# Optimization experiments

Measured on AMD Instinct MI355X. Metric: run time of the kernel, lower is better.

## Reference

```python
import jax, jax.numpy as jnp
import numpy as np

FEAT = 256
HID = 256
HEADS = 4
DH = HID // HEADS
SCALE = DH ** (-0.5)


def _linear(x, W, b):
    # torch nn.Linear convention: W is [out, in]
    return jnp.einsum('...i,oi->...o', x, W) + b


def _layernorm(x, gamma, beta, eps=1e-5):
    mu = jnp.mean(x, axis=-1, keepdims=True)
    var = jnp.mean(jnp.square(x - mu), axis=-1, keepdims=True)
    return (x - mu) * jax.lax.rsqrt(var + eps) * gamma + beta


def setup_inputs() -> dict:
    key = jax.random.key(0)
    ks = jax.random.split(key, 16)
    B, N = 4, 2048
    def w(k, shape, fan_in):
        return jax.random.uniform(k, shape, jnp.float32, -1.0, 1.0) / np.sqrt(fan_in)
    return {
        'x0': jax.random.normal(ks[0], (B, N, FEAT), jnp.float32),
        'x1': jax.random.normal(ks[1], (B, N, FEAT), jnp.float32),
        'Wqk': w(ks[2], (HID, FEAT), FEAT), 'bqk': w(ks[3], (HID,), FEAT),
        'Wv': w(ks[4], (HID, FEAT), FEAT), 'bv': w(ks[5], (HID,), FEAT),
        'Wp': w(ks[6], (HID, HID), HID), 'bp': w(ks[7], (HID,), HID),
        'W1': w(ks[8], (FEAT * 2, FEAT + HID), FEAT + HID), 'b1': w(ks[9], (FEAT * 2,), FEAT + HID),
        'gamma': jnp.ones((FEAT * 2,), jnp.float32), 'beta': jnp.zeros((FEAT * 2,), jnp.float32),
        'W2': w(ks[10], (FEAT, FEAT * 2), FEAT * 2), 'b2': w(ks[11], (FEAT,), FEAT * 2),
    }


def _forward(x0, x1, Wqk, bqk, Wv, bv, Wp, bp, W1, b1, gamma, beta, W2, b2):
    B, N0, _ = x0.shape
    N1 = x1.shape[1]

    def heads(t):  # [B, N, HID] -> [B, H, N, DH]
        return t.reshape(t.shape[0], t.shape[1], HEADS, DH).transpose(0, 2, 1, 3)

    qk0 = heads(_linear(x0, Wqk, bqk)) * (SCALE ** 0.5)
    qk1 = heads(_linear(x1, Wqk, bqk)) * (SCALE ** 0.5)
    v0 = heads(_linear(x0, Wv, bv))
    v1 = heads(_linear(x1, Wv, bv))

    sim = jnp.einsum('bhid,bhjd->bhij', qk0, qk1)  # [B,H,N0,N1]
    attn01 = jax.nn.softmax(sim, axis=-1)                      # rows over N1
    attn10 = jax.nn.softmax(sim.transpose(0, 1, 3, 2), axis=-1)  # [B,H,N1,N0], rows over N0

    m0 = jnp.einsum('bhij,bhjd->bhid', attn01, v1)  # [B,H,N0,DH]
    m1 = jnp.einsum('bhij,bhjd->bhid', attn10, v0)  # [B,H,N1,DH]

    def merge(t):  # [B,H,N,DH] -> [B,N,HID]
        return t.transpose(0, 2, 1, 3).reshape(t.shape[0], t.shape[2], HID)

    m0 = _linear(merge(m0), Wp, bp)
    m1 = _linear(merge(m1), Wp, bp)

    def mlp(x, m):
        h = _linear(jnp.concatenate([x, m], axis=-1), W1, b1)
        h = jax.nn.gelu(_layernorm(h, gamma, beta), approximate=False)
        return x + _linear(h, W2, b2)

    return mlp(x0, m0), mlp(x1, m1)


def reference(x0, x1, Wqk, bqk, Wv, bv, Wp, bp, W1, b1, gamma, beta, W2, b2):
    return _forward(x0, x1, Wqk, bqk, Wv, bv, Wp, bp, W1, b1, gamma, beta, W2, b2)
```

## Files before the change

### kernel.cpp

```cpp
#include <hip/hip_runtime.h>
#include <hip/hip_bf16.h>
#include <math.h>

typedef __hip_bfloat16 hbf;
typedef __attribute__((ext_vector_type(8))) short short8;
typedef __attribute__((ext_vector_type(4))) short short4v;
typedef __attribute__((ext_vector_type(4))) float f32x4;

#define ROWS 8192
#define SQSL 0.4246609001440095f
#define COFF 24.0f

__device__ __forceinline__ short f2b(float f) {
    union { hbf h; short s; } u; u.h = __float2bfloat16(f); return u.s;
}
__device__ __forceinline__ float b2f(short s) {
    union { unsigned u; float f; } x;
    x.u = ((unsigned)(unsigned short)s) << 16; return x.f;
}

__global__ __launch_bounds__(256)
void prep(const float* __restrict__ x0, const float* __restrict__ x1,
          const float* __restrict__ Wqk, const float* __restrict__ Wv,
          const float* __restrict__ Wp, const float* __restrict__ W1,
          const float* __restrict__ W2,
          const float* __restrict__ bp, const float* __restrict__ b1,
          short* __restrict__ xbf, short* __restrict__ wq,
          short* __restrict__ wv, short* __restrict__ w1c,
          short* __restrict__ w2, float* __restrict__ bc)
{
    const int bid = blockIdx.x, tid = threadIdx.x;
    if (bid < 4608) {
        if (bid >= 4224 && bid < 4480) {
            int i = (bid - 4224) * 256 + tid;
            int n = i >> 7, c = (i & 127) * 4;
            if (c < 256) {
                float4 f = ((const float4*)W1)[i];
                short4v s;
                s[0] = f2b(f.x); s[1] = f2b(f.y); s[2] = f2b(f.z); s[3] = f2b(f.w);
                *(short4v*)(w1c + (size_t)n * 512 + c) = s;
            }
            return;
        }
        const float* src; short* dst; int base; float sc = 1.f;
        if (bid < 2048)      { src = x0;  dst = xbf;              base = bid; }
        else if (bid < 4096) { src = x1;  dst = xbf + 8192 * 256; base = bid - 2048; }
        else if (bid < 4160) { src = Wqk; dst = wq; base = bid - 4096; sc = SQSL; }
        else if (bid < 4224) { src = Wv;  dst = wv; base = bid - 4160; }
        else                 { src = W2;  dst = w2; base = bid - 4480; }
        int i = base * 256 + tid;
        float4 f = ((const float4*)src)[i];
        short4v s;
        s[0] = f2b(f.x * sc); s[1] = f2b(f.y * sc);
        s[2] = f2b(f.z * sc); s[3] = f2b(f.w * sc);
        *(short4v*)(dst + (size_t)i * 4) = s;
    } else if (bid < 5120) {
        int n = bid - 4608;
        const float* wrow = W1 + (size_t)n * 512 + 256;
        float acc = 0.f;
        for (int k = 0; k < 256; ++k)
            acc += wrow[k] * Wp[(size_t)k * 256 + tid];
        w1c[(size_t)n * 512 + 256 + tid] = f2b(acc);
    } else {
        int n = (bid - 5120) * 256 + tid;
        const float* wrow = W1 + (size_t)n * 512 + 256;
        float acc = b1[n];
        for (int k = 0; k < 256; ++k) acc += wrow[k] * bp[k];
        bc[n] = acc;
    }
}

__global__ __launch_bounds__(256)
void gemm_qkv(const short* __restrict__ A0,
              const short* __restrict__ Wa, const short* __restrict__ Wb,
              const float* __restrict__ bias0, const float* __restrict__ bias1,
              short* __restrict__ Cb, short* __restrict__ Cb2)
{
    const int col0 = blockIdx.x * 128;
    const int row0 = blockIdx.y * 64;
    const int tid = threadIdx.x;
    const int lane = tid & 63, wave = tid >> 6;
    const int ln = lane & 15, quad = lane >> 4;
    const int wm = wave & 1, wn = wave >> 1;

    __shared__ short As[64 * 40];
    __shared__ short Bs[128 * 40];

    const int ar = tid >> 2, ac = tid & 3;

    f32x4 acc[2][4];
    #pragma unroll
    for (int i = 0; i < 2; ++i)
        #pragma unroll
        for (int j = 0; j < 4; ++j) acc[i][j] = {0.f, 0.f, 0.f, 0.f};

    auto wptr = [&](int rr, int kk) -> const short* {
        int n = col0 + rr;
        if (col0 < 256) return Wa + (size_t)n * 256 + kk;
        return Wb + (size_t)(n - 256) * 256 + kk;
    };

    short8 aR  = *(const short8*)(A0 + (size_t)(row0 + ar) * 256 + ac * 8);
    short8 bR0 = *(const short8*)wptr(ar, ac * 8);
    short8 bR1 = *(const short8*)wptr(ar + 64, ac * 8);

    for (int k0 = 0; k0 < 256; k0 += 32) {
        *(short8*)&As[ar * 40 + ac * 8] = aR;
        *(short8*)&Bs[ar * 40 + ac * 8] = bR0;
        *(short8*)&Bs[(ar + 64) * 40 + ac * 8] = bR1;
        __syncthreads();

        if (k0 + 32 < 256) {
            aR  = *(const short8*)(A0 + (size_t)(row0 + ar) * 256 + k0 + 32 + ac * 8);
            bR0 = *(const short8*)wptr(ar, k0 + 32 + ac * 8);
            bR1 = *(const short8*)wptr(ar + 64, k0 + 32 + ac * 8);
        }

        short8 a[2], b[4];
        #pragma unroll
        for (int mi = 0; mi < 2; ++mi)
            a[mi] = *(const short8*)&As[(wm * 32 + mi * 16 + ln) * 40 + quad * 8];
        #pragma unroll
        for (int nj = 0; nj < 4; ++nj)
            b[nj] = *(const short8*)&Bs[(wn * 64 + nj * 16 + ln) * 40 + quad * 8];
        #pragma unroll
        for (int mi = 0; mi < 2; ++mi)
            #pragma unroll
            for (int nj = 0; nj < 4; ++nj)
                acc[mi][nj] = __builtin_amdgcn_mfma_f32_16x16x32_bf16(
                                  b[nj], a[mi], acc[mi][nj], 0, 0, 0);
        __syncthreads();
    }

    #pragma unroll
    for (int nj = 0; nj < 4; ++nj) {
        int wrel = wn * 64 + nj * 16 + quad * 4;
        int wcol = col0 + wrel;
        const float* bias = (wcol >= 256) ? bias1 : bias0;
        int boff = (wcol >= 256) ? (wcol - 256) : wcol;
        float4 bb = *(const float4*)(bias + boff);
        #pragma unroll
        for (int mi = 0; mi < 2; ++mi) {
            int tok = row0 + wm * 32 + mi * 16 + ln;
            f32x4 v = acc[mi][nj];
            short4v o;
            if (wcol < 256) {
                o[0] = f2b(fmaf(bb.x, SQSL, v[0])); o[1] = f2b(fmaf(bb.y, SQSL, v[1]));
                o[2] = f2b(fmaf(bb.z, SQSL, v[2])); o[3] = f2b(fmaf(bb.w, SQSL, v[3]));
                *(short4v*)(Cb + (size_t)tok * 256 + wcol) = o;
            } else {
                o[0] = f2b(v[0] + bb.x); o[1] = f2b(v[1] + bb.y);
                o[2] = f2b(v[2] + bb.z); o[3] = f2b(v[3] + bb.w);
                *(short4v*)(Cb2 + (size_t)tok * 256 + (wcol - 256)) = o;
            }
        }
    }
}

__global__ __launch_bounds__(256)
void vtrans(const short* __restrict__ vbuf, short* __restrict__ vtbuf)
{
    const int tt = blockIdx.x;
    const int gh = blockIdx.y;
    const int g = gh >> 2, h = gh & 3;
    const int tid = threadIdx.x;
    const int tok0 = g * 2048 + tt * 64;

    __shared__ short Ls[64 * 76];

    {
        int c4 = tid & 15, r0 = tid >> 4;
        #pragma unroll
        for (int gg = 0; gg < 4; ++gg) {
            int r = r0 + gg * 16;
            *(short4v*)&Ls[r * 76 + c4 * 4] =
                *(const short4v*)(vbuf + (size_t)(tok0 + r) * 256 + h * 64 + c4 * 4);
        }
    }
    __syncthreads();

    #pragma unroll
    for (int p = 0; p < 2; ++p) {
        int ch = tid + p * 256;
        int d = ch >> 3, cc = ch & 7;
        short8 s;
        #pragma unroll
        for (int j = 0; j < 8; ++j) s[j] = Ls[(cc * 8 + j) * 76 + d];
        *(short8*)(vtbuf + (size_t)((g * 4 + h) * 64 + d) * 2048 + tt * 64 + cc * 8) = s;
    }
}

__global__ __launch_bounds__(256)
void attn7(const short* __restrict__ qkb, const short* __restrict__ vtbuf,
           short* __restrict__ pO0, short* __restrict__ pO1,
           float* __restrict__ l0, float* __restrict__ l1)
{
    const int qt   = blockIdx.x;
    const int b    = blockIdx.y >> 2, h = blockIdx.y & 3;
    const int dir  = blockIdx.z >> 1;
    const int half = blockIdx.z & 1;
    const int tid = threadIdx.x;
    const int lane = tid & 63, wave = tid >> 6;
    const int ln   = lane & 15, quad = lane >> 4;

    const int qbase = dir * ROWS + b * 2048;
    const int kbase = (1 - dir) * ROWS + b * 2048;
    const int vg    = ((1 - dir) * 4 + b) * 4 + h;
    const int jlo   = half * 1024, jhi = jlo + 1024;

    short* __restrict__ pO = half ? pO1 : pO0;
    float* __restrict__ lb = half ? l1  : l0;

    __shared__ short QP[128 * 72];
    __shared__ short KS[64 * 72];
    __shared__ short VT[64 * 72];

    const int c = tid & 7, r0 = tid >> 3;
    #pragma unroll
    for (int g = 0; g < 4; ++g) {
        int r = r0 + g * 32;
        *(short8*)&QP[r * 72 + c * 8] =
            *(const short8*)(qkb + (size_t)(qbase + qt * 128 + r) * 256 + h * 64 + c * 8);
    }
    #pragma unroll
    for (int g = 0; g < 2; ++g) {
        int r = r0 + g * 32;
        *(short8*)&KS[r * 72 + c * 8] =
            *(const short8*)(qkb + (size_t)(kbase + jlo + r) * 256 + h * 64 + c * 8);
        *(short8*)&VT[r * 72 + c * 8] =
            *(const short8*)(vtbuf + (size_t)(vg * 64 + r) * 2048 + jlo + c * 8);
    }
    __syncthreads();

    short8 qf[2][2];
    #pragma unroll
    for (int mi = 0; mi < 2; ++mi)
        #pragma unroll
        for (int ks = 0; ks < 2; ++ks)
            qf[mi][ks] = *(const short8*)&QP[(wave * 32 + mi * 16 + ln) * 72
                                             + ks * 32 + quad * 8];

    f32x4 Ot[2][4];
    #pragma unroll
    for (int mi = 0; mi < 2; ++mi)
        #pragma unroll
        for (int dt = 0; dt < 4; ++dt) Ot[mi][dt] = {0.f, 0.f, 0.f, 0.f};
    float lrun[2] = {0.f, 0.f};

    for (int j0 = jlo; j0 < jhi; j0 += 64) {
        short8 kreg[2], vreg[2];
        const bool more = (j0 + 64) < jhi;
        if (more) {
            #pragma unroll
            for (int g = 0; g < 2; ++g) {
                int r = r0 + g * 32;
                kreg[g] = *(const short8*)(qkb + (size_t)(kbase + j0 + 64 + r) * 256
                                           + h * 64 + c * 8);
                vreg[g] = *(const short8*)(vtbuf + (size_t)(vg * 64 + r) * 2048
                                           + j0 + 64 + c * 8);
            }
        }

        f32x4 St[2][4];
        #pragma unroll
        for (int t = 0; t < 4; ++t) {
            short8 k0 = *(const short8*)&KS[(t * 16 + ln) * 72 + quad * 8];
            short8 k1 = *(const short8*)&KS[(t * 16 + ln) * 72 + 32 + quad * 8];
            #pragma unroll
            for (int mi = 0; mi < 2; ++mi) {
                f32x4 z = {0.f, 0.f, 0.f, 0.f};
                z = __builtin_amdgcn_mfma_f32_16x16x32_bf16(k0, qf[mi][0], z, 0, 0, 0);
                St[mi][t] = __builtin_amdgcn_mfma_f32_16x16x32_bf16(k1, qf[mi][1], z, 0, 0, 0);
            }
        }

        float ss[2] = {0.f, 0.f};
        #pragma unroll
        for (int mi = 0; mi < 2; ++mi)
            #pragma unroll
            for (int t = 0; t < 4; ++t) {
                float p0 = __builtin_amdgcn_exp2f(St[mi][t][0] - COFF);
                float p1 = __builtin_amdgcn_exp2f(St[mi][t][1] - COFF);
                float p2 = __builtin_amdgcn_exp2f(St[mi][t][2] - COFF);
                float p3 = __builtin_amdgcn_exp2f(St[mi][t][3] - COFF);
                ss[mi] += (p0 + p1) + (p2 + p3);
                unsigned d0 = (__float_as_uint(p0) >> 16) |
                              (__float_as_uint(p1) & 0xffff0000u);
                unsigned d1 = (__float_as_uint(p2) >> 16) |
                              (__float_as_uint(p3) & 0xffff0000u);
                *(int2*)&QP[(wave * 32 + mi * 16 + ln) * 72 + t * 16 + quad * 4] =
                    make_int2((int)d0, (int)d1);
            }
        #pragma unroll
        for (int mi = 0; mi < 2; ++mi) {
            float t = ss[mi];
            t += __shfl_xor(t, 16);
            t += __shfl_xor(t, 32);
            lrun[mi] += t;
        }

        short8 pa[2][2];
        #pragma unroll
        for (int mi = 0; mi < 2; ++mi)
            #pragma unroll
            for (int ks = 0; ks < 2; ++ks)
                pa[mi][ks] = *(const short8*)&QP[(wave * 32 + mi * 16 + ln) * 72
                                                 + ks * 32 + quad * 8];
        #pragma unroll
        for (int dt = 0; dt < 4; ++dt) {
            short8 v0 = *(const short8*)&VT[(dt * 16 + ln) * 72 + quad * 8];
            short8 v1 = *(const short8*)&VT[(dt * 16 + ln) * 72 + 32 + quad * 8];
            #pragma unroll
            for (int mi = 0; mi < 2; ++mi) {
                Ot[mi][dt] = __builtin_amdgcn_mfma_f32_16x16x32_bf16(
                                 v0, pa[mi][0], Ot[mi][dt], 0, 0, 0);
                Ot[mi][dt] = __builtin_amdgcn_mfma_f32_16x16x32_bf16(
                                 v1, pa[mi][1], Ot[mi][dt], 0, 0, 0);
            }
        }
        __syncthreads();

        if (more) {
            #pragma unroll
            for (int g = 0; g < 2; ++g) {
                int r = r0 + g * 32;
                *(short8*)&KS[r * 72 + c * 8] = kreg[g];
                *(short8*)&VT[r * 72 + c * 8] = vreg[g];
            }
        }
        __syncthreads();
    }

    #pragma unroll
    for (int mi = 0; mi < 2; ++mi) {
        int tok = qbase + qt * 128 + wave * 32 + mi * 16 + ln;
        if (quad == 0) lb[tok] = lrun[mi];
        #pragma unroll
        for (int dt = 0; dt < 4; ++dt) {
            short4v o;
            #pragma unroll
            for (int r = 0; r < 4; ++r) o[r] = f2b(Ot[mi][dt][r]);
            *(short4v*)(pO + (size_t)tok * 256 + h * 64 + dt * 16 + quad * 4) = o;
        }
    }
}

__global__ __launch_bounds__(256)
void mlp_fused(const short* __restrict__ xbf,
               const short* __restrict__ pO0, const short* __restrict__ pO1,
               const float* __restrict__ l0, const float* __restrict__ l1,
               const short* __restrict__ w1c, const short* __restrict__ w2,
               const float* __restrict__ bc, const float* __restrict__ gamma,
               const float* __restrict__ beta, const float* __restrict__ b2,
               const float* __restrict__ x0, const float* __restrict__ x1,
               float* __restrict__ out)
{
    const int tok0 = blockIdx.x * 32;
    const int tid = threadIdx.x;
    const int lane = tid & 63, wave = tid >> 6;
    const int ln = lane & 15, quad = lane >> 4;

    __shared__ short As[32 * 40];
    __shared__ short Bs[256 * 40];
    __shared__ short H [32 * 520];
    __shared__ float stats[4][2][32];

    f32x4 acc[2][8];
    #pragma unroll
    for (int i = 0; i < 2; ++i)
        #pragma unroll
        for (int j = 0; j < 8; ++j) acc[i][j] = {0.f, 0.f, 0.f, 0.f};

    const int br = tid >> 2, bcol = tid & 3;

    for (int k0 = 0; k0 < 512; k0 += 32) {
        #pragma unroll
        for (int p = 0; p < 2; ++p) {
            if (p == 0 && tid < 128) {
                int arow = tid >> 2, ac = tid & 3;
                int kk = k0 + ac * 8;
                int tok = tok0 + arow;
                short8 s;
                if (k0 < 256) {
                    s = *(const short8*)(xbf + (size_t)tok * 256 + kk);
                } else {
                    short8 a = *(const short8*)(pO0 + (size_t)tok * 256 + (kk - 256));
                    short8 b = *(const short8*)(pO1 + (size_t)tok * 256 + (kk - 256));
                    float inv = __builtin_amdgcn_rcpf(l0[tok] + l1[tok]);
                    #pragma unroll
                    for (int j = 0; j < 8; ++j)
                        s[j] = f2b((b2f(a[j]) + b2f(b[j])) * inv);
                }
                *(short8*)&As[arow * 40 + ac * 8] = s;
            }
            #pragma unroll
            for (int q = 0; q < 4; ++q) {
                int r = br + q * 64;
                *(short8*)&Bs[r * 40 + bcol * 8] =
                    *(const short8*)(w1c + (size_t)(p * 256 + r) * 512 + k0 + bcol * 8);
            }
            __syncthreads();

            short8 a0 = *(const short8*)&As[ln * 40 + quad * 8];
            short8 a1 = *(const short8*)&As[(16 + ln) * 40 + quad * 8];
            #pragma unroll
            for (int nj = 0; nj < 4; ++nj) {
                short8 bf = *(const short8*)&Bs[(wave * 64 + nj * 16 + ln) * 40 + quad * 8];
                acc[0][p * 4 + nj] = __builtin_amdgcn_mfma_f32_16x16x32_bf16(
                                         bf, a0, acc[0][p * 4 + nj], 0, 0, 0);
                acc[1][p * 4 + nj] = __builtin_amdgcn_mfma_f32_16x16x32_bf16(
                                         bf, a1, acc[1][p * 4 + nj], 0, 0, 0);
            }
            __syncthreads();
        }
    }

    #pragma unroll
    for (int p = 0; p < 2; ++p)
        #pragma unroll
        for (int nj = 0; nj < 4; ++nj) {
            int hcol = p * 256 + wave * 64 + nj * 16 + quad * 4;
            float4 bb = *(const float4*)(bc + hcol);
            acc[0][p * 4 + nj][0] += bb.x; acc[1][p * 4 + nj][0] += bb.x;
            acc[0][p * 4 + nj][1] += bb.y; acc[1][p * 4 + nj][1] += bb.y;
            acc[0][p * 4 + nj][2] += bb.z; acc[1][p * 4 + nj][2] += bb.z;
            acc[0][p * 4 + nj][3] += bb.w; acc[1][p * 4 + nj][3] += bb.w;
        }

    #pragma unroll
    for (int mi = 0; mi < 2; ++mi) {
        float s1 = 0.f, s2 = 0.f;
        #pragma unroll
        for (int j = 0; j < 8; ++j)
            #pragma unroll
            for (int r = 0; r < 4; ++r) {
                float v = acc[mi][j][r];
                s1 += v; s2 += v * v;
            }
        s1 += __shfl_xor(s1, 16); s2 += __shfl_xor(s2, 16);
        s1 += __shfl_xor(s1, 32); s2 += __shfl_xor(s2, 32);
        if (quad == 0) {
            stats[wave][0][mi * 16 + ln] = s1;
            stats[wave][1][mi * 16 + ln] = s2;
        }
    }
    __syncthreads();

    float mean[2], rstd[2];
    #pragma unroll
    for (int mi = 0; mi < 2; ++mi) {
        int t = mi * 16 + ln;
        float s1 = stats[0][0][t] + stats[1][0][t] + stats[2][0][t] + stats[3][0][t];
        float s2 = stats[0][1][t] + stats[1][1][t] + stats[2][1][t] + stats[3][1][t];
        mean[mi] = s1 * (1.f / 512.f);
        float var = s2 * (1.f / 512.f) - mean[mi] * mean[mi];
        rstd[mi] = rsqrtf(var + 1e-5f);
    }

    #pragma unroll
    for (int p = 0; p < 2; ++p)
        #pragma unroll
        for (int nj = 0; nj < 4; ++nj) {
            int hcol = p * 256 + wave * 64 + nj * 16 + quad * 4;
            float4 gm = *(const float4*)(gamma + hcol);
            float4 bt = *(const float4*)(beta + hcol);
            #pragma unroll
            for (int mi = 0; mi < 2; ++mi) {
                short4v o;
                #pragma unroll
                for (int r = 0; r < 4; ++r) {
                    float g = (r == 0) ? gm.x : (r == 1) ? gm.y : (r == 2) ? gm.z : gm.w;
                    float bta = (r == 0) ? bt.x : (r == 1) ? bt.y : (r == 2) ? bt.z : bt.w;
                    float y = (acc[mi][p * 4 + nj][r] - mean[mi]) * rstd[mi] * g + bta;
                    float u = y * fmaf(y * y, 0.0356774081f, 0.7978845608f);
                    float e = __builtin_amdgcn_exp2f(u * -2.8853900818f);
                    o[r] = f2b(y * __builtin_amdgcn_rcpf(1.f + e));
                }
                *(short4v*)&H[(mi * 16 + ln) * 520 + hcol] = o;
            }
        }
    __syncthreads();

    f32x4 acc2[2][4];
    #pragma unroll
    for (int i = 0; i < 2; ++i)
        #pragma unroll
        for (int j = 0; j < 4; ++j) acc2[i][j] = {0.f, 0.f, 0.f, 0.f};

    for (int k0 = 0; k0 < 512; k0 += 32) {
        #pragma unroll
        for (int q = 0; q < 4; ++q) {
            int r = br + q * 64;
            *(short8*)&Bs[r * 40 + bcol * 8] =
                *(const short8*)(w2 + (size_t)r * 512 + k0 + bcol * 8);
        }
        __syncthreads();

        short8 h0 = *(const short8*)&H[ln * 520 + k0 + quad * 8];
        short8 h1 = *(const short8*)&H[(16 + ln) * 520 + k0 + quad * 8];
        #pragma unroll
        for (int nj = 0; nj < 4; ++nj) {
            short8 wf = *(const short8*)&Bs[(wave * 64 + nj * 16 + ln) * 40 + quad * 8];
            acc2[0][nj] = __builtin_amdgcn_mfma_f32_16x16x32_bf16(wf, h0, acc2[0][nj], 0, 0, 0);
            acc2[1][nj] = __builtin_amdgcn_mfma_f32_16x16x32_bf16(wf, h1, acc2[1][nj], 0, 0, 0);
        }
        __syncthreads();
    }

    #pragma unroll
    for (int nj = 0; nj < 4; ++nj) {
        int ocol = wave * 64 + nj * 16 + quad * 4;
        float4 bb = *(const float4*)(b2 + ocol);
        #pragma unroll
        for (int mi = 0; mi < 2; ++mi) {
            int tok = tok0 + mi * 16 + ln;
            const float* xr = (tok < ROWS ? x0 + (size_t)tok * 256
                                          : x1 + (size_t)(tok - ROWS) * 256);
            float4 rv = *(const float4*)(xr + ocol);
            float4 o;
            o.x = acc2[mi][nj][0] + bb.x + rv.x;
            o.y = acc2[mi][nj][1] + bb.y + rv.y;
            o.z = acc2[mi][nj][2] + bb.z + rv.z;
            o.w = acc2[mi][nj][3] + bb.w + rv.w;
            *(float4*)(out + (size_t)tok * 256 + ocol) = o;
        }
    }
}

extern "C" void kernel_launch(void* const* d_in, const int* in_sizes, int n_in,
                              void* d_out, int out_size, void* d_ws, size_t ws_size,
                              hipStream_t stream)
{
    const float* x0    = (const float*)d_in[0];
    const float* x1    = (const float*)d_in[1];
    const float* Wqk   = (const float*)d_in[2];
    const float* bqk   = (const float*)d_in[3];
    const float* Wv    = (const float*)d_in[4];
    const float* bv    = (const float*)d_in[5];
    const float* Wp    = (const float*)d_in[6];
    const float* bp    = (const float*)d_in[7];
    const float* W1    = (const float*)d_in[8];
    const float* b1    = (const float*)d_in[9];
    const float* gamma = (const float*)d_in[10];
    const float* beta  = (const float*)d_in[11];
    const float* W2    = (const float*)d_in[12];
    const float* b2    = (const float*)d_in[13];
    float* out = (float*)d_out;

    char* ws = (char*)d_ws;
    const size_t MB = 1024 * 1024;
    short* xbf  = (short*)ws;
    short* qkb  = (short*)(ws + 8  * MB);
    short* vtb  = (short*)(ws + 16 * MB);
    short* pO0  = (short*)(ws + 24 * MB);
    short* pO1  = (short*)(ws + 32 * MB);
    short* vbuf = pO1;
    float* l0   = (float*)(ws + 40 * MB);
    float* l1   = l0 + 16384;
    float* bc   = l1 + 16384;
    short* wq   = (short*)(bc + 512);
    short* wv   = wq + 65536;
    short* w1c  = wv + 65536;
    short* w2   = w1c + 262144;

    prep<<<5122, 256, 0, stream>>>(x0, x1, Wqk, Wv, Wp, W1, W2, bp, b1,
                                   xbf, wq, wv, w1c, w2, bc);
    gemm_qkv<<<dim3(4, 256), 256, 0, stream>>>(xbf, wq, wv, bqk, bv, qkb, vbuf);
    vtrans<<<dim3(32, 32), 256, 0, stream>>>(vbuf, vtb);
    attn7<<<dim3(16, 16, 4), 256, 0, stream>>>(qkb, vtb, pO0, pO1, l0, l1);
    mlp_fused<<<512, 256, 0, stream>>>(xbf, pO0, pO1, l0, l1, w1c, w2, bc,
                                       gamma, beta, b2, x0, x1, out);
}
```

Baseline: 224.4 us.

## Fuse fp32-to-bf16 input conversion into GEMMs and use two-wave attention blocks

After: 221.0 us. No clear change (-1.5%).

```diff
diff --git a/kernel.cpp b/kernel.cpp
--- a/kernel.cpp
+++ b/kernel.cpp
@@ -20,19 +20,21 @@
 }
 
 __global__ __launch_bounds__(256)
-void prep(const float* __restrict__ x0, const float* __restrict__ x1,
-          const float* __restrict__ Wqk, const float* __restrict__ Wv,
+void prep(const float* __restrict__ Wqk, const float* __restrict__ Wv,
           const float* __restrict__ Wp, const float* __restrict__ W1,
           const float* __restrict__ W2,
           const float* __restrict__ bp, const float* __restrict__ b1,
-          short* __restrict__ xbf, short* __restrict__ wq,
-          short* __restrict__ wv, short* __restrict__ w1c,
-          short* __restrict__ w2, float* __restrict__ bc)
+          short* __restrict__ wq, short* __restrict__ wv,
+          short* __restrict__ w1c, short* __restrict__ w2,
+          float* __restrict__ bc)
 {
     const int bid = blockIdx.x, tid = threadIdx.x;
-    if (bid < 4608) {
-        if (bid >= 4224 && bid < 4480) {
-            int i = (bid - 4224) * 256 + tid;
+    if (bid < 512) {
+        const float* src; short* dst; int base; float sc = 1.f;
+        if (bid < 64)       { src = Wqk; dst = wq; base = bid;       sc = SQSL; }
+        else if (bid < 128) { src = Wv;  dst = wv; base = bid - 64; }
+        else if (bid < 384) {
+            int i = (bid - 128) * 256 + tid;
             int n = i >> 7, c = (i & 127) * 4;
             if (c < 256) {
                 float4 f = ((const float4*)W1)[i];
@@ -42,27 +44,22 @@
             }
             return;
         }
-        const float* src; short* dst; int base; float sc = 1.f;
-        if (bid < 2048)      { src = x0;  dst = xbf;              base = bid; }
-        else if (bid < 4096) { src = x1;  dst = xbf + 8192 * 256; base = bid - 2048; }
-        else if (bid < 4160) { src = Wqk; dst = wq; base = bid - 4096; sc = SQSL; }
-        else if (bid < 4224) { src = Wv;  dst = wv; base = bid - 4160; }
-        else                 { src = W2;  dst = w2; base = bid - 4480; }
+        else                { src = W2;  dst = w2; base = bid - 384; }
         int i = base * 256 + tid;
         float4 f = ((const float4*)src)[i];
         short4v s;
         s[0] = f2b(f.x * sc); s[1] = f2b(f.y * sc);
         s[2] = f2b(f.z * sc); s[3] = f2b(f.w * sc);
         *(short4v*)(dst + (size_t)i * 4) = s;
-    } else if (bid < 5120) {
-        int n = bid - 4608;
+    } else if (bid < 1024) {
+        int n = bid - 512;
         const float* wrow = W1 + (size_t)n * 512 + 256;
         float acc = 0.f;
         for (int k = 0; k < 256; ++k)
             acc += wrow[k] * Wp[(size_t)k * 256 + tid];
         w1c[(size_t)n * 512 + 256 + tid] = f2b(acc);
     } else {
-        int n = (bid - 5120) * 256 + tid;
+        int n = (bid - 1024) * 256 + tid;
         const float* wrow = W1 + (size_t)n * 512 + 256;
         float acc = b1[n];
         for (int k = 0; k < 256; ++k) acc += wrow[k] * bp[k];
@@ -71,7 +68,7 @@
 }
 
 __global__ __launch_bounds__(256)
-void gemm_qkv(const short* __restrict__ A0,
+void gemm_qkv(const float* __restrict__ x0, const float* __restrict__ x1,
               const short* __restrict__ Wa, const short* __restrict__ Wb,
               const float* __restrict__ bias0, const float* __restrict__ bias1,
               short* __restrict__ Cb, short* __restrict__ Cb2)
@@ -99,19 +96,29 @@
         if (col0 < 256) return Wa + (size_t)n * 256 + kk;
         return Wb + (size_t)(n - 256) * 256 + kk;
     };
-
-    short8 aR  = *(const short8*)(A0 + (size_t)(row0 + ar) * 256 + ac * 8);
+    const float* xrow = (row0 + ar < ROWS)
+        ? x0 + (size_t)(row0 + ar) * 256
+        : x1 + (size_t)(row0 + ar - ROWS) * 256;
+
+    float4 aF0 = ((const float4*)(xrow + ac * 8))[0];
+    float4 aF1 = ((const float4*)(xrow + ac * 8))[1];
     short8 bR0 = *(const short8*)wptr(ar, ac * 8);
     short8 bR1 = *(const short8*)wptr(ar + 64, ac * 8);
 
     for (int k0 = 0; k0 < 256; k0 += 32) {
-        *(short8*)&As[ar * 40 + ac * 8] = aR;
+        {
+            short8 s;
+            s[0] = f2b(aF0.x); s[1] = f2b(aF0.y); s[2] = f2b(aF0.z); s[3] = f2b(aF0.w);
+            s[4] = f2b(aF1.x); s[5] = f2b(aF1.y); s[6] = f2b(aF1.z); s[7] = f2b(aF1.w);
+            *(short8*)&As[ar * 40 + ac * 8] = s;
+        }
         *(short8*)&Bs[ar * 40 + ac * 8] = bR0;
         *(short8*)&Bs[(ar + 64) * 40 + ac * 8] = bR1;
         __syncthreads();
 
         if (k0 + 32 < 256) {
-            aR  = *(const short8*)(A0 + (size_t)(row0 + ar) * 256 + k0 + 32 + ac * 8);
+            aF0 = ((const float4*)(xrow + k0 + 32 + ac * 8))[0];
+            aF1 = ((const float4*)(xrow + k0 + 32 + ac * 8))[1];
             bR0 = *(const short8*)wptr(ar, k0 + 32 + ac * 8);
             bR1 = *(const short8*)wptr(ar + 64, k0 + 32 + ac * 8);
         }
@@ -190,8 +197,8 @@
     }
 }
 
-__global__ __launch_bounds__(256)
-void attn7(const short* __restrict__ qkb, const short* __restrict__ vtbuf,
+__global__ __launch_bounds__(128, 2)
+void attn8(const short* __restrict__ qkb, const short* __restrict__ vtbuf,
            short* __restrict__ pO0, short* __restrict__ pO1,
            float* __restrict__ l0, float* __restrict__ l1)
 {
@@ -217,14 +224,14 @@
 
     const int c = tid & 7, r0 = tid >> 3;
     #pragma unroll
-    for (int g = 0; g < 4; ++g) {
-        int r = r0 + g * 32;
+    for (int g = 0; g < 8; ++g) {
+        int r = r0 + g * 16;
         *(short8*)&QP[r * 72 + c * 8] =
             *(const short8*)(qkb + (size_t)(qbase + qt * 128 + r) * 256 + h * 64 + c * 8);
     }
     #pragma unroll
-    for (int g = 0; g < 2; ++g) {
-        int r = r0 + g * 32;
+    for (int g = 0; g < 4; ++g) {
+        int r = r0 + g * 16;
         *(short8*)&KS[r * 72 + c * 8] =
             *(const short8*)(qkb + (size_t)(kbase + jlo + r) * 256 + h * 64 + c * 8);
         *(short8*)&VT[r * 72 + c * 8] =
@@ -232,28 +239,28 @@
     }
     __syncthreads();
 
-    short8 qf[2][2];
-    #pragma unroll
-    for (int mi = 0; mi < 2; ++mi)
+    short8 qf[4][2];
+    #pragma unroll
+    for (int mi = 0; mi < 4; ++mi)
         #pragma unroll
         for (int ks = 0; ks < 2; ++ks)
-            qf[mi][ks] = *(const short8*)&QP[(wave * 32 + mi * 16 + ln) * 72
+            qf[mi][ks] = *(const short8*)&QP[(wave * 64 + mi * 16 + ln) * 72
                                              + ks * 32 + quad * 8];
 
-    f32x4 Ot[2][4];
-    #pragma unroll
-    for (int mi = 0; mi < 2; ++mi)
+    f32x4 Ot[4][4];
+    #pragma unroll
+    for (int mi = 0; mi < 4; ++mi)
         #pragma unroll
         for (int dt = 0; dt < 4; ++dt) Ot[mi][dt] = {0.f, 0.f, 0.f, 0.f};
-    float lrun[2] = {0.f, 0.f};
+    float lrun[4] = {0.f, 0.f, 0.f, 0.f};
 
     for (int j0 = jlo; j0 < jhi; j0 += 64) {
-        short8 kreg[2], vreg[2];
+        short8 kreg[4], vreg[4];
         const bool more = (j0 + 64) < jhi;
         if (more) {
             #pragma unroll
-            for (int g = 0; g < 2; ++g) {
-                int r = r0 + g * 32;
+            for (int g = 0; g < 4; ++g) {
+                int r = r0 + g * 16;
                 kreg[g] = *(const short8*)(qkb + (size_t)(kbase + j0 + 64 + r) * 256
                                            + h * 64 + c * 8);
                 vreg[g] = *(const short8*)(vtbuf + (size_t)(vg * 64 + r) * 2048
@@ -261,22 +268,22 @@
             }
         }
 
-        f32x4 St[2][4];
+        f32x4 St[4][4];
         #pragma unroll
         for (int t = 0; t < 4; ++t) {
             short8 k0 = *(const short8*)&KS[(t * 16 + ln) * 72 + quad * 8];
             short8 k1 = *(const short8*)&KS[(t * 16 + ln) * 72 + 32 + quad * 8];
             #pragma unroll
-            for (int mi = 0; mi < 2; ++mi) {
+            for (int mi = 0; mi < 4; ++mi) {
                 f32x4 z = {0.f, 0.f, 0.f, 0.f};
                 z = __builtin_amdgcn_mfma_f32_16x16x32_bf16(k0, qf[mi][0], z, 0, 0, 0);
                 St[mi][t] = __builtin_amdgcn_mfma_f32_16x16x32_bf16(k1, qf[mi][1], z, 0, 0, 0);
             }
         }
 
-        float ss[2] = {0.f, 0.f};
-        #pragma unroll
-        for (int mi = 0; mi < 2; ++mi)
+        float ss[4] = {0.f, 0.f, 0.f, 0.f};
+        #pragma unroll
+        for (int mi = 0; mi < 4; ++mi)
             #pragma unroll
             for (int t = 0; t < 4; ++t) {
                 float p0 = __builtin_amdgcn_exp2f(St[mi][t][0] - COFF);
@@ -288,30 +295,30 @@
                               (__float_as_uint(p1) & 0xffff0000u);
                 unsigned d1 = (__float_as_uint(p2) >> 16) |
                               (__float_as_uint(p3) & 0xffff0000u);
-                *(int2*)&QP[(wave * 32 + mi * 16 + ln) * 72 + t * 16 + quad * 4] =
+                *(int2*)&QP[(wave * 64 + mi * 16 + ln) * 72 + t * 16 + quad * 4] =
                     make_int2((int)d0, (int)d1);
             }
         #pragma unroll
-        for (int mi = 0; mi < 2; ++mi) {
+        for (int mi = 0; mi < 4; ++mi) {
             float t = ss[mi];
             t += __shfl_xor(t, 16);
             t += __shfl_xor(t, 32);
             lrun[mi] += t;
         }
 
-        short8 pa[2][2];
-        #pragma unroll
-        for (int mi = 0; mi < 2; ++mi)
+        short8 pa[4][2];
+        #pragma unroll
+        for (int mi = 0; mi < 4; ++mi)
             #pragma unroll
             for (int ks = 0; ks < 2; ++ks)
-                pa[mi][ks] = *(const short8*)&QP[(wave * 32 + mi * 16 + ln) * 72
+                pa[mi][ks] = *(const short8*)&QP[(wave * 64 + mi * 16 + ln) * 72
                                                  + ks * 32 + quad * 8];
         #pragma unroll
         for (int dt = 0; dt < 4; ++dt) {
             short8 v0 = *(const short8*)&VT[(dt * 16 + ln) * 72 + quad * 8];
             short8 v1 = *(const short8*)&VT[(dt * 16 + ln) * 72 + 32 + quad * 8];
             #pragma unroll
-            for (int mi = 0; mi < 2; ++mi) {
+            for (int mi = 0; mi < 4; ++mi) {
                 Ot[mi][dt] = __builtin_amdgcn_mfma_f32_16x16x32_bf16(
                                  v0, pa[mi][0], Ot[mi][dt], 0, 0, 0);
                 Ot[mi][dt] = __builtin_amdgcn_mfma_f32_16x16x32_bf16(
@@ -322,8 +329,8 @@
 
         if (more) {
             #pragma unroll
-            for (int g = 0; g < 2; ++g) {
-                int r = r0 + g * 32;
+            for (int g = 0; g < 4; ++g) {
+                int r = r0 + g * 16;
                 *(short8*)&KS[r * 72 + c * 8] = kreg[g];
                 *(short8*)&VT[r * 72 + c * 8] = vreg[g];
             }
@@ -332,8 +339,8 @@
     }
 
     #pragma unroll
-    for (int mi = 0; mi < 2; ++mi) {
-        int tok = qbase + qt * 128 + wave * 32 + mi * 16 + ln;
+    for (int mi = 0; mi < 4; ++mi) {
+        int tok = qbase + qt * 128 + wave * 64 + mi * 16 + ln;
         if (quad == 0) lb[tok] = lrun[mi];
         #pragma unroll
         for (int dt = 0; dt < 4; ++dt) {
@@ -346,13 +353,12 @@
 }
 
 __global__ __launch_bounds__(256)
-void mlp_fused(const short* __restrict__ xbf,
+void mlp_fused(const float* __restrict__ x0, const float* __restrict__ x1,
                const short* __restrict__ pO0, const short* __restrict__ pO1,
                const float* __restrict__ l0, const float* __restrict__ l1,
                const short* __restrict__ w1c, const short* __restrict__ w2,
                const float* __restrict__ bc, const float* __restrict__ gamma,
                const float* __restrict__ beta, const float* __restrict__ b2,
-               const float* __restrict__ x0, const float* __restrict__ x1,
                float* __restrict__ out)
 {
     const int tok0 = blockIdx.x * 32;
@@ -382,7 +388,12 @@
                 int tok = tok0 + arow;
                 short8 s;
                 if (k0 < 256) {
-                    s = *(const short8*)(xbf + (size_t)tok * 256 + kk);
+                    const float* xr = (tok < ROWS ? x0 + (size_t)tok * 256
+                                                  : x1 + (size_t)(tok - ROWS) * 256) + kk;
+                    float4 f0 = ((const float4*)xr)[0];
+                    float4 f1 = ((const float4*)xr)[1];
+                    s[0] = f2b(f0.x); s[1] = f2b(f0.y); s[2] = f2b(f0.z); s[3] = f2b(f0.w);
+                    s[4] = f2b(f1.x); s[5] = f2b(f1.y); s[6] = f2b(f1.z); s[7] = f2b(f1.w);
                 } else {
                     short8 a = *(const short8*)(pO0 + (size_t)tok * 256 + (kk - 256));
                     short8 b = *(const short8*)(pO1 + (size_t)tok * 256 + (kk - 256));
@@ -549,13 +560,12 @@
 
     char* ws = (char*)d_ws;
     const size_t MB = 1024 * 1024;
-    short* xbf  = (short*)ws;
-    short* qkb  = (short*)(ws + 8  * MB);
-    short* vtb  = (short*)(ws + 16 * MB);
-    short* pO0  = (short*)(ws + 24 * MB);
-    short* pO1  = (short*)(ws + 32 * MB);
+    short* qkb  = (short*)ws;
+    short* vtb  = (short*)(ws + 8  * MB);
+    short* pO0  = (short*)(ws + 16 * MB);
+    short* pO1  = (short*)(ws + 24 * MB);
     short* vbuf = pO1;
-    float* l0   = (float*)(ws + 40 * MB);
+    float* l0   = (float*)(ws + 32 * MB);
     float* l1   = l0 + 16384;
     float* bc   = l1 + 16384;
     short* wq   = (short*)(bc + 512);
@@ -563,11 +573,11 @@
     short* w1c  = wv + 65536;
     short* w2   = w1c + 262144;
 
-    prep<<<5122, 256, 0, stream>>>(x0, x1, Wqk, Wv, Wp, W1, W2, bp, b1,
-                                   xbf, wq, wv, w1c, w2, bc);
-    gemm_qkv<<<dim3(4, 256), 256, 0, stream>>>(xbf, wq, wv, bqk, bv, qkb, vbuf);
+    prep<<<1026, 256, 0, stream>>>(Wqk, Wv, Wp, W1, W2, bp, b1,
+                                   wq, wv, w1c, w2, bc);
+    gemm_qkv<<<dim3(4, 256), 256, 0, stream>>>(x0, x1, wq, wv, bqk, bv, qkb, vbuf);
     vtrans<<<dim3(32, 32), 256, 0, stream>>>(vbuf, vtb);
-    attn7<<<dim3(16, 16, 4), 256, 0, stream>>>(qkb, vtb, pO0, pO1, l0, l1);
-    mlp_fused<<<512, 256, 0, stream>>>(xbf, pO0, pO1, l0, l1, w1c, w2, bc,
-                                       gamma, beta, b2, x0, x1, out);
-}
+    attn8<<<dim3(16, 16, 4), 128, 0, stream>>>(qkb, vtb, pO0, pO1, l0, l1);
+    mlp_fused<<<512, 256, 0, stream>>>(x0, x1, pO0, pO1, l0, l1, w1c, w2, bc,
+                                       gamma, beta, b2, out);
+}
```
